# Optimization experiments

Hardware: AMD Instinct MI355X
Metric: run time of the kernel (lower is better)

## Reference

```python
import jax, jax.numpy as jnp
from jax import lax
import numpy as np

DEPTH, SRC, TRG, B, H = 2, 32, 32, 32, 256


def setup_inputs() -> dict:
    key = jax.random.key(0)
    ks = jax.random.split(key, 5)
    s = 1.0 / np.sqrt(H)
    return {
        "source": jax.random.normal(ks[0], (SRC, B, H), jnp.float32),
        "target": jax.random.normal(ks[1], (TRG, B, H), jnp.float32),
        "W": jax.random.uniform(ks[2], (DEPTH, H, H), jnp.float32, -s, s),
        "U": jax.random.uniform(ks[3], (DEPTH, 2 * H, H), jnp.float32, -s, s),
        "b": jax.random.uniform(ks[4], (DEPTH, 1, H), jnp.float32, -s, s),
    }


def _grid_rnn(source, target, W, U, b):
    depth = W.shape[0]
    src_len, batch, hid = source.shape
    trg_len = target.shape[0]
    dt = source.dtype
    # Layer-0 inputs: x_t = source[i] (broadcast over j), y_t = target[j] (broadcast over i)
    x_in = jnp.broadcast_to(source[:, None], (src_len, trg_len, batch, hid))
    y_in = jnp.broadcast_to(target[None, :], (src_len, trg_len, batch, hid))
    outs = []
    for d in range(depth):
        Wd, bd = W[d], b[d]
        Ux, Uy = U[d][:hid], U[d][hid:]  # state = concat([state_x, state_y])
        # Precompute input projections: x_t @ W, y_t @ W for all (i,j)
        Xp = jnp.einsum('ijbh,hk->ijbk', x_in, Wd)
        Yp = jnp.einsum('ijbh,hk->ijbk', y_in, Wd)

        def cell_step(prev_hx, inputs):
            xp, yp, sx = inputs  # sx = h_x from row above (state_x)
            temp = sx @ Ux + prev_hx @ Uy + bd
            hx = jnp.tanh(xp + temp)
            hy = jnp.tanh(yp + temp)
            return hx, (hx, hy)

        def row_step(prev_row_hx, row_in):
            xp_row, yp_row = row_in  # [trg, B, H]
            _, (hx_row, hy_row) = lax.scan(
                cell_step, jnp.zeros((batch, hid), dt), (xp_row, yp_row, prev_row_hx))
            return hx_row, (hx_row, hy_row)

        _, (HX, HY) = lax.scan(row_step, jnp.zeros((trg_len, batch, hid), dt), (Xp, Yp))
        outs.append(jnp.stack([HX, HY], axis=2))  # [src, trg, 2, B, H]
        x_in, y_in = HX, HY  # next layer reads h_output[d-1,i,j,0/1]
    return jnp.stack(outs, 0)  # [depth, src, trg, 2, B, H]


def reference(source, target, W, U, b):
    return _grid_rnn(source, target, W, U, b)
```

## Files before the change

### kernel.cpp

```cpp
#include <hip/hip_runtime.h>
#include <math.h>

#define SRCN 32
#define TRGN 32
#define BN   32
#define HN   256
#define BH   (BN*HN)
#define CELL (2*BH)
#define DSZ  ((size_t)SRCN*TRGN*CELL)
#define NRB  8
#define NBS  4

__host__ __device__ __forceinline__ int ncd(int t) {
    int a = t + 1, b = 63 - t;
    int m = a < b ? a : b;
    return m < 32 ? m : 32;
}

__device__ __forceinline__ void spinwait(int* p) {
    for (int n = 0; n < (1 << 20); ++n) {
        if (__hip_atomic_fetch_add(p, 0, __ATOMIC_RELAXED, __HIP_MEMORY_SCOPE_AGENT) > 0)
            return;
        __builtin_amdgcn_s_sleep(2);
    }
}
__device__ __forceinline__ float cldf(const float* p) {
    return __hip_atomic_load(p, __ATOMIC_RELAXED, __HIP_MEMORY_SCOPE_AGENT);
}
__device__ __forceinline__ void cstf(float* p, float v) {
    __hip_atomic_store(p, v, __ATOMIC_RELAXED, __HIP_MEMORY_SCOPE_AGENT);
}

__global__ __launch_bounds__(256) void proj0_kernel(
    const float* __restrict__ src, const float* __restrict__ trg,
    const float* __restrict__ W0, float* __restrict__ Xp0, float* __restrict__ Yp0)
{
    __shared__ float xs[BH];
    int blk = blockIdx.x >> 2, tile = blockIdx.x & 3;
    const float* X; float* P;
    if (blk < SRCN) { X = src + blk * BH; P = Xp0 + blk * BH; }
    else            { X = trg + (blk - SRCN) * BH; P = Yp0 + (blk - SRCN) * BH; }
    int tid = threadIdx.x;
    { const float4* x4 = (const float4*)X; float4* s4 = (float4*)xs;
#pragma unroll
      for (int r = 0; r < 8; ++r) s4[tid + r * 256] = x4[tid + r * 256]; }
    __syncthreads();
    int h = tile * 64 + (tid & 63), bg = tid >> 6;
    float acc[8] = {0,0,0,0,0,0,0,0};
    for (int k = 0; k < HN; k += 4) {
        float w0 = W0[(k+0)*HN+h], w1 = W0[(k+1)*HN+h], w2 = W0[(k+2)*HN+h], w3 = W0[(k+3)*HN+h];
#pragma unroll
        for (int bb = 0; bb < 8; ++bb) {
            int b = bg * 8 + bb;
            float4 xv = *(const float4*)&xs[b * HN + k];
            acc[bb] += xv.x*w0 + xv.y*w1 + xv.z*w2 + xv.w*w3;
        }
    }
#pragma unroll
    for (int bb = 0; bb < 8; ++bb) P[(bg*8+bb)*HN + h] = acc[bb];
}

__global__ __launch_bounds__(512, 1) void chain3_kernel(
    const float* __restrict__ W, const float* __restrict__ U,
    const float* __restrict__ bias, float* __restrict__ out,
    const float* __restrict__ xp0, const float* __restrict__ yp0,
    int* __restrict__ flg)
{
    __shared__ __align__(16) float sPrev[NRB][HN];
    __shared__ __align__(16) float sUp[NRB][HN];
    __shared__ __align__(16) float sX0[NRB][HN];
    __shared__ __align__(16) float sY0[NRB][HN];
    __shared__ __align__(16) float redT[NRB][HN];
    __shared__ __align__(16) float redX[NRB][HN];
    __shared__ __align__(16) float redY[NRB][HN];

    const int blk = blockIdx.x;
    const int L   = blk >> 7;
    const int i   = (blk >> 2) & 31;
    const int bs  = blk & (NBS - 1);
    const int r0  = bs * NRB;
    const int tid = threadIdx.x;
    const int h   = tid & 255;
    const int kh  = tid >> 8;
    const int kof = kh * 128;

    const float* UxB = U + (size_t)L * 131072 + (size_t)kof * HN + h;
    const float* UyB = UxB + 65536;
    const float* W1B = W + 65536 + (size_t)kof * HN + h;
    const float bv   = bias[L * HN + h];
    float* outL = out + (size_t)L * DSZ;
    int* flgL   = flg + L * 4096;

#pragma unroll
    for (int bb = 0; bb < 4; ++bb) sPrev[kh * 4 + bb][h] = 0.f;
    __syncthreads();

    for (int j = 0; j < TRGN; ++j) {
        const int cell = i * TRGN + j;

        if (L == 1) {
            if (tid == 0) spinwait(&flg[cell * NBS + bs]);
            __syncthreads();
            const float* x0 = out + (size_t)cell * CELL + (size_t)r0 * HN + h;
#pragma unroll
            for (int bb = 0; bb < 4; ++bb) {
                int b = kh * 4 + bb;
                sX0[b][h] = cldf(x0 + b * HN);
                sY0[b][h] = cldf(x0 + BH + b * HN);
            }
            __syncthreads();
        }

        float acc[NRB] = {0.f,0.f,0.f,0.f,0.f,0.f,0.f,0.f};
        if (j > 0) {
#pragma unroll 2
            for (int k = 0; k < 128; k += 4) {
                float w0 = UyB[(k+0)*HN], w1 = UyB[(k+1)*HN];
                float w2 = UyB[(k+2)*HN], w3 = UyB[(k+3)*HN];
#pragma unroll
                for (int b = 0; b < NRB; ++b) {
                    float4 s = *(const float4*)&sPrev[b][kof + k];
                    acc[b] += s.x*w0 + s.y*w1 + s.z*w2 + s.w*w3;
                }
            }
        }
        float aX[NRB] = {0.f,0.f,0.f,0.f,0.f,0.f,0.f,0.f};
        float aY[NRB] = {0.f,0.f,0.f,0.f,0.f,0.f,0.f,0.f};
        float xin[NRB], yin[NRB];
        if (L == 1) {
#pragma unroll 2
            for (int k = 0; k < 128; k += 4) {
                float w0 = W1B[(k+0)*HN], w1 = W1B[(k+1)*HN];
                float w2 = W1B[(k+2)*HN], w3 = W1B[(k+3)*HN];
#pragma unroll
                for (int b = 0; b < NRB; ++b) {
                    float4 sx4 = *(const float4*)&sX0[b][kof + k];
                    float4 sy4 = *(const float4*)&sY0[b][kof + k];
                    aX[b] += sx4.x*w0 + sx4.y*w1 + sx4.z*w2 + sx4.w*w3;
                    aY[b] += sy4.x*w0 + sy4.y*w1 + sy4.z*w2 + sy4.w*w3;
                }
            }
        } else if (kh == 0) {
            const float* xr = xp0 + (size_t)i * BH + (size_t)r0 * HN + h;
            const float* yr = yp0 + (size_t)j * BH + (size_t)r0 * HN + h;
#pragma unroll
            for (int b = 0; b < NRB; ++b) {
                xin[b] = xr[b * HN];
                yin[b] = yr[b * HN];
            }
        }

        if (tid == 0 && i > 0) spinwait(&flgL[((i - 1) * 32 + j) * NBS + bs]);
        __syncthreads();
        if (i > 0) {
            const float* up = outL + (size_t)((i - 1) * TRGN + j) * CELL
                            + (size_t)r0 * HN + h;
#pragma unroll
            for (int bb = 0; bb < 4; ++bb) {
                int b = kh * 4 + bb;
                sUp[b][h] = cldf(up + b * HN);
            }
            __syncthreads();
#pragma unroll 2
            for (int k = 0; k < 128; k += 4) {
                float w0 = UxB[(k+0)*HN], w1 = UxB[(k+1)*HN];
                float w2 = UxB[(k+2)*HN], w3 = UxB[(k+3)*HN];
#pragma unroll
                for (int b = 0; b < NRB; ++b) {
                    float4 s = *(const float4*)&sUp[b][kof + k];
                    acc[b] += s.x*w0 + s.y*w1 + s.z*w2 + s.w*w3;
                }
            }
        }

        if (kh == 1) {
#pragma unroll
            for (int b = 0; b < NRB; ++b) {
                redT[b][h] = acc[b];
                if (L == 1) { redX[b][h] = aX[b]; redY[b][h] = aY[b]; }
            }
        }
        __syncthreads();

        float temp[NRB];
        if (kh == 0) {
            float* ox = outL + (size_t)cell * CELL + (size_t)r0 * HN + h;
            if (L == 0) {
#pragma unroll
                for (int b = 0; b < NRB; ++b) {
                    float tp = acc[b] + redT[b][h] + bv;
                    float hx = tanhf(xin[b] + tp);
                    float hy = tanhf(yin[b] + tp);
                    cstf(ox + b * HN, hx);
                    cstf(ox + BH + b * HN, hy);
                    sPrev[b][h] = hx;
                }
            } else {
#pragma unroll
                for (int b = 0; b < NRB; ++b) {
                    float tp = acc[b] + redT[b][h] + bv;
                    temp[b] = tp;
                    float hx = tanhf(aX[b] + redX[b][h] + tp);
                    cstf(ox + b * HN, hx);
                    sPrev[b][h] = hx;
                }
            }
        }
        __syncthreads();
        if (tid == 0)
            __hip_atomic_fetch_add(&flgL[cell * NBS + bs], 1,
                                   __ATOMIC_RELEASE, __HIP_MEMORY_SCOPE_AGENT);

        if (L == 1 && kh == 0) {
            float* oy = outL + (size_t)cell * CELL + BH + (size_t)r0 * HN + h;
#pragma unroll
            for (int b = 0; b < NRB; ++b)
                oy[b * HN] = tanhf(aY[b] + redY[b][h] + temp[b]);
        }
    }
}

__global__ __launch_bounds__(256) void proj1_kernel(
    float* __restrict__ out, const float* __restrict__ W1)
{
    __shared__ float hxs[BH];
    __shared__ float hys[BH];
    int cell = blockIdx.x >> 2, tile = blockIdx.x & 3;
    const float* hx0 = out + (size_t)cell * CELL;
    const float* hy0 = hx0 + BH;
    float* xp1 = out + DSZ + (size_t)cell * CELL;
    float* yp1 = xp1 + BH;
    int tid = threadIdx.x;
    { const float4* a4 = (const float4*)hx0; const float4* b4 = (const float4*)hy0;
      float4* sa = (float4*)hxs; float4* sb = (float4*)hys;
#pragma unroll
      for (int r = 0; r < 8; ++r) { sa[tid+r*256] = a4[tid+r*256]; sb[tid+r*256] = b4[tid+r*256]; } }
    __syncthreads();
    int h = tile * 64 + (tid & 63), bg = tid >> 6;
    float ax[8] = {0,0,0,0,0,0,0,0}, ay[8] = {0,0,0,0,0,0,0,0};
    for (int k = 0; k < HN; k += 4) {
        float w0 = W1[(k+0)*HN+h], w1 = W1[(k+1)*HN+h], w2 = W1[(k+2)*HN+h], w3 = W1[(k+3)*HN+h];
#pragma unroll
        for (int bb = 0; bb < 8; ++bb) {
            int b = bg * 8 + bb;
            float4 xv = *(const float4*)&hxs[b*HN+k];
            float4 yv = *(const float4*)&hys[b*HN+k];
            ax[bb] += xv.x*w0 + xv.y*w1 + xv.z*w2 + xv.w*w3;
            ay[bb] += yv.x*w0 + yv.y*w1 + yv.z*w2 + yv.w*w3;
        }
    }
#pragma unroll
    for (int bb = 0; bb < 8; ++bb) {
        int b = bg * 8 + bb;
        xp1[b*HN+h] = ax[bb]; yp1[b*HN+h] = ay[bb];
    }
}

__global__ __launch_bounds__(256) void diag_kernel(
    float* out, const float* __restrict__ U, const float* __restrict__ bias,
    const float* __restrict__ Xp0, const float* __restrict__ Yp0, int d, int t)
{
    __shared__ float sxs[BH];
    __shared__ float phs[BH];
    int c = blockIdx.x >> 2, tile = blockIdx.x & 3;
    int i0 = t - (TRGN - 1); if (i0 < 0) i0 = 0;
    int i = i0 + c, j = t - i;
    const float* Ux = U + d * (2 * HN * HN);
    const float* Uy = Ux + HN * HN;
    float* outD = out + (size_t)d * DSZ;
    const float* sx = (i > 0) ? outD + (size_t)((i-1)*TRGN + j) * CELL : nullptr;
    const float* ph = (j > 0) ? outD + (size_t)(i*TRGN + (j-1)) * CELL : nullptr;
    float* oHX = outD + (size_t)(i*TRGN + j) * CELL;
    float* oHY = oHX + BH;
    const float* xp = d ? oHX : (Xp0 + i * BH);
    const float* yp = d ? oHY : (Yp0 + j * BH);
    const float* bd = bias + d * HN;
    int tid = threadIdx.x;
    { const float4* s4 = (const float4*)sx; const float4* p4 = (const float4*)ph;
      float4* d1 = (float4*)sxs; float4* d2 = (float4*)phs;
      float4 z = make_float4(0.f,0.f,0.f,0.f);
#pragma unroll
      for (int r = 0; r < 8; ++r) { int idx = tid + r*256; d1[idx] = sx ? s4[idx] : z; d2[idx] = ph ? p4[idx] : z; } }
    __syncthreads();
    int h = tile * 64 + (tid & 63), bg = tid >> 6;
    float acc[8] = {0,0,0,0,0,0,0,0};
    for (int k = 0; k < HN; k += 4) {
        float ux0 = Ux[(k+0)*HN+h], ux1 = Ux[(k+1)*HN+h], ux2 = Ux[(k+2)*HN+h], ux3 = Ux[(k+3)*HN+h];
        float uy0 = Uy[(k+0)*HN+h], uy1 = Uy[(k+1)*HN+h], uy2 = Uy[(k+2)*HN+h], uy3 = Uy[(k+3)*HN+h];
#pragma unroll
        for (int bb = 0; bb < 8; ++bb) {
            int b = bg * 8 + bb;
            float4 sv = *(const float4*)&sxs[b*HN+k];
            float4 pv = *(const float4*)&phs[b*HN+k];
            acc[bb] += sv.x*ux0 + sv.y*ux1 + sv.z*ux2 + sv.w*ux3
                     + pv.x*uy0 + pv.y*uy1 + pv.z*uy2 + pv.w*uy3;
        }
    }
    float bv = bd[h];
#pragma unroll
    for (int bb = 0; bb < 8; ++bb) {
        int b = bg * 8 + bb;
        float temp = acc[bb] + bv;
        oHX[b*HN+h] = tanhf(xp[b*HN+h] + temp);
        oHY[b*HN+h] = tanhf(yp[b*HN+h] + temp);
    }
}

extern "C" void kernel_launch(void* const* d_in, const int* in_sizes, int n_in,
                              void* d_out, int out_size, void* d_ws, size_t ws_size,
                              hipStream_t stream)
{
    const float* source = (const float*)d_in[0];
    const float* target = (const float*)d_in[1];
    const float* W      = (const float*)d_in[2];
    const float* U      = (const float*)d_in[3];
    const float* bias   = (const float*)d_in[4];
    float* out = (float*)d_out;

    const size_t need = 2u * 1024 * 1024 + 32768;
    if (d_ws != nullptr && ws_size >= need) {
        float* xp0 = (float*)d_ws;
        float* yp0 = xp0 + 32 * BH;
        int*   flg = (int*)(yp0 + 32 * BH);
        hipMemsetAsync(flg, 0, 2 * 32 * 32 * NBS * sizeof(int), stream);
        proj0_kernel<<<dim3(64 * 4), dim3(256), 0, stream>>>(source, target, W, xp0, yp0);
        chain3_kernel<<<dim3(2 * 32 * NBS), dim3(512), 0, stream>>>(
            W, U, bias, out, xp0, yp0, flg);
    } else {
        float* Xp0 = out + DSZ;
        float* Yp0 = Xp0 + SRCN * BH;
        proj0_kernel<<<dim3(64 * 4), dim3(256), 0, stream>>>(source, target, W, Xp0, Yp0);
        for (int t = 0; t < SRCN + TRGN - 1; ++t) {
            int nc = ncd(t);
            diag_kernel<<<dim3(nc * 4), dim3(256), 0, stream>>>(out, U, bias, Xp0, Yp0, 0, t);
        }
        proj1_kernel<<<dim3(1024 * 4), dim3(256), 0, stream>>>(out, W + HN * HN);
        for (int t = 0; t < SRCN + TRGN - 1; ++t) {
            int nc = ncd(t);
            diag_kernel<<<dim3(nc * 4), dim3(256), 0, stream>>>(out, U, bias, nullptr, nullptr, 1, t);
        }
    }
}
```

Baseline: 1.582 ms.

## Split layer-1 input projection into dedicated producer blocks in persistent kernel

Adds a third group of 128 blocks that compute the layer-1 input projections (W1 applied to layer-0 hx/hy) per cell and publish them via a new flag array. Layer-1 recurrence blocks then just load the precomputed projections instead of doing the W1 matmul on their critical path. The projection work moves off the serial diagonal chain, at the cost of more resident blocks, an extra round trip through global memory, and another spin-wait per cell.

```diff
diff --git a/kernel.cpp b/kernel.cpp
--- a/kernel.cpp
+++ b/kernel.cpp
@@ -60,56 +60,92 @@
     for (int bb = 0; bb < 8; ++bb) P[(bg*8+bb)*HN + h] = acc[bb];
 }
 
-__global__ __launch_bounds__(512, 1) void chain3_kernel(
+__global__ __launch_bounds__(512, 1) void chain4_kernel(
     const float* __restrict__ W, const float* __restrict__ U,
     const float* __restrict__ bias, float* __restrict__ out,
     const float* __restrict__ xp0, const float* __restrict__ yp0,
     int* __restrict__ flg)
 {
-    __shared__ __align__(16) float sPrev[NRB][HN];
-    __shared__ __align__(16) float sUp[NRB][HN];
-    __shared__ __align__(16) float sX0[NRB][HN];
-    __shared__ __align__(16) float sY0[NRB][HN];
-    __shared__ __align__(16) float redT[NRB][HN];
-    __shared__ __align__(16) float redX[NRB][HN];
-    __shared__ __align__(16) float redY[NRB][HN];
-
-    const int blk = blockIdx.x;
-    const int L   = blk >> 7;
-    const int i   = (blk >> 2) & 31;
-    const int bs  = blk & (NBS - 1);
-    const int r0  = bs * NRB;
-    const int tid = threadIdx.x;
-    const int h   = tid & 255;
-    const int kh  = tid >> 8;
-    const int kof = kh * 128;
-
+    __shared__ __align__(16) float sA[NRB][HN];
+    __shared__ __align__(16) float sB[NRB][HN];
+    __shared__ __align__(16) float sC[NRB][HN];
+    __shared__ __align__(16) float sD[NRB][HN];
+
+    const int role = blockIdx.x >> 7;
+    const int i    = (blockIdx.x >> 2) & 31;
+    const int bs   = blockIdx.x & 3;
+    const int r0   = bs * NRB;
+    const int tid  = threadIdx.x;
+    const int h    = tid & 255;
+    const int kh   = tid >> 8;
+    const int kof  = kh * 128;
+
+    int* flgL0 = flg;
+    int* p1f   = flg + 4096;
+    int* flgL1 = flg + 8192;
+
+    if (role == 1) {
+        const float* W1B = W + 65536 + (size_t)kof * HN + h;
+        for (int j = 0; j < TRGN; ++j) {
+            const int cell = i * TRGN + j;
+            if (tid == 0) spinwait(&flgL0[cell * NBS + bs]);
+            __syncthreads();
+            const float* x0 = out + (size_t)cell * CELL + (size_t)r0 * HN + h;
+#pragma unroll
+            for (int bb = 0; bb < 4; ++bb) {
+                int b = kh * 4 + bb;
+                sA[b][h] = cldf(x0 + b * HN);
+                sB[b][h] = cldf(x0 + BH + b * HN);
+            }
+            __syncthreads();
+            float aX[NRB] = {0.f,0.f,0.f,0.f,0.f,0.f,0.f,0.f};
+            float aY[NRB] = {0.f,0.f,0.f,0.f,0.f,0.f,0.f,0.f};
+#pragma unroll 2
+            for (int k = 0; k < 128; k += 4) {
+                float w0 = W1B[(k+0)*HN], w1 = W1B[(k+1)*HN];
+                float w2 = W1B[(k+2)*HN], w3 = W1B[(k+3)*HN];
+#pragma unroll
+                for (int b = 0; b < NRB; ++b) {
+                    float4 sx4 = *(const float4*)&sA[b][kof + k];
+                    float4 sy4 = *(const float4*)&sB[b][kof + k];
+                    aX[b] += sx4.x*w0 + sx4.y*w1 + sx4.z*w2 + sx4.w*w3;
+                    aY[b] += sy4.x*w0 + sy4.y*w1 + sy4.z*w2 + sy4.w*w3;
+                }
+            }
+            if (kh == 1) {
+#pragma unroll
+                for (int b = 0; b < NRB; ++b) { sC[b][h] = aX[b]; sD[b][h] = aY[b]; }
+            }
+            __syncthreads();
+            if (kh == 0) {
+                float* xd = out + DSZ + (size_t)cell * CELL + (size_t)r0 * HN + h;
+#pragma unroll
+                for (int b = 0; b < NRB; ++b) {
+                    cstf(xd + b * HN,      aX[b] + sC[b][h]);
+                    cstf(xd + BH + b * HN, aY[b] + sD[b][h]);
+                }
+            }
+            __syncthreads();
+            if (tid == 0)
+                __hip_atomic_fetch_add(&p1f[cell * NBS + bs], 1,
+                                       __ATOMIC_RELEASE, __HIP_MEMORY_SCOPE_AGENT);
+        }
+        return;
+    }
+
+    const int L = (role == 2);
     const float* UxB = U + (size_t)L * 131072 + (size_t)kof * HN + h;
     const float* UyB = UxB + 65536;
-    const float* W1B = W + 65536 + (size_t)kof * HN + h;
     const float bv   = bias[L * HN + h];
     float* outL = out + (size_t)L * DSZ;
-    int* flgL   = flg + L * 4096;
-
-#pragma unroll
-    for (int bb = 0; bb < 4; ++bb) sPrev[kh * 4 + bb][h] = 0.f;
+    int* myf    = L ? flgL1 : flgL0;
+
+#pragma unroll
+    for (int bb = 0; bb < 4; ++bb) sA[kh * 4 + bb][h] = 0.f;
     __syncthreads();
 
     for (int j = 0; j < TRGN; ++j) {
         const int cell = i * TRGN + j;
-
-        if (L == 1) {
-            if (tid == 0) spinwait(&flg[cell * NBS + bs]);
-            __syncthreads();
-            const float* x0 = out + (size_t)cell * CELL + (size_t)r0 * HN + h;
-#pragma unroll
-            for (int bb = 0; bb < 4; ++bb) {
-                int b = kh * 4 + bb;
-                sX0[b][h] = cldf(x0 + b * HN);
-                sY0[b][h] = cldf(x0 + BH + b * HN);
-            }
-            __syncthreads();
-        }
 
         float acc[NRB] = {0.f,0.f,0.f,0.f,0.f,0.f,0.f,0.f};
         if (j > 0) {
@@ -119,46 +155,39 @@
                 float w2 = UyB[(k+2)*HN], w3 = UyB[(k+3)*HN];
 #pragma unroll
                 for (int b = 0; b < NRB; ++b) {
-                    float4 s = *(const float4*)&sPrev[b][kof + k];
+                    float4 s = *(const float4*)&sA[b][kof + k];
                     acc[b] += s.x*w0 + s.y*w1 + s.z*w2 + s.w*w3;
                 }
             }
         }
-        float aX[NRB] = {0.f,0.f,0.f,0.f,0.f,0.f,0.f,0.f};
-        float aY[NRB] = {0.f,0.f,0.f,0.f,0.f,0.f,0.f,0.f};
         float xin[NRB], yin[NRB];
-        if (L == 1) {
-#pragma unroll 2
-            for (int k = 0; k < 128; k += 4) {
-                float w0 = W1B[(k+0)*HN], w1 = W1B[(k+1)*HN];
-                float w2 = W1B[(k+2)*HN], w3 = W1B[(k+3)*HN];
-#pragma unroll
-                for (int b = 0; b < NRB; ++b) {
-                    float4 sx4 = *(const float4*)&sX0[b][kof + k];
-                    float4 sy4 = *(const float4*)&sY0[b][kof + k];
-                    aX[b] += sx4.x*w0 + sx4.y*w1 + sx4.z*w2 + sx4.w*w3;
-                    aY[b] += sy4.x*w0 + sy4.y*w1 + sy4.z*w2 + sy4.w*w3;
-                }
-            }
-        } else if (kh == 0) {
+        if (!L && kh == 0) {
             const float* xr = xp0 + (size_t)i * BH + (size_t)r0 * HN + h;
             const float* yr = yp0 + (size_t)j * BH + (size_t)r0 * HN + h;
 #pragma unroll
+            for (int b = 0; b < NRB; ++b) { xin[b] = xr[b * HN]; yin[b] = yr[b * HN]; }
+        }
+
+        if (tid == 0) {
+            if (L)     spinwait(&p1f[cell * NBS + bs]);
+            if (i > 0) spinwait(&myf[((i - 1) * 32 + j) * NBS + bs]);
+        }
+        __syncthreads();
+        if (L && kh == 0) {
+            const float* xd = out + DSZ + (size_t)cell * CELL + (size_t)r0 * HN + h;
+#pragma unroll
             for (int b = 0; b < NRB; ++b) {
-                xin[b] = xr[b * HN];
-                yin[b] = yr[b * HN];
-            }
-        }
-
-        if (tid == 0 && i > 0) spinwait(&flgL[((i - 1) * 32 + j) * NBS + bs]);
-        __syncthreads();
+                xin[b] = cldf(xd + b * HN);
+                yin[b] = cldf(xd + BH + b * HN);
+            }
+        }
         if (i > 0) {
             const float* up = outL + (size_t)((i - 1) * TRGN + j) * CELL
                             + (size_t)r0 * HN + h;
 #pragma unroll
             for (int bb = 0; bb < 4; ++bb) {
                 int b = kh * 4 + bb;
-                sUp[b][h] = cldf(up + b * HN);
+                sB[b][h] = cldf(up + b * HN);
             }
             __syncthreads();
 #pragma unroll 2
@@ -167,7 +196,7 @@
                 float w2 = UxB[(k+2)*HN], w3 = UxB[(k+3)*HN];
 #pragma unroll
                 for (int b = 0; b < NRB; ++b) {
-                    float4 s = *(const float4*)&sUp[b][kof + k];
+                    float4 s = *(const float4*)&sB[b][kof + k];
                     acc[b] += s.x*w0 + s.y*w1 + s.z*w2 + s.w*w3;
                 }
             }
@@ -175,48 +204,26 @@
 
         if (kh == 1) {
 #pragma unroll
-            for (int b = 0; b < NRB; ++b) {
-                redT[b][h] = acc[b];
-                if (L == 1) { redX[b][h] = aX[b]; redY[b][h] = aY[b]; }
-            }
+            for (int b = 0; b < NRB; ++b) sC[b][h] = acc[b];
         }
         __syncthreads();
-
-        float temp[NRB];
         if (kh == 0) {
             float* ox = outL + (size_t)cell * CELL + (size_t)r0 * HN + h;
-            if (L == 0) {
-#pragma unroll
-                for (int b = 0; b < NRB; ++b) {
-                    float tp = acc[b] + redT[b][h] + bv;
-                    float hx = tanhf(xin[b] + tp);
-                    float hy = tanhf(yin[b] + tp);
-                    cstf(ox + b * HN, hx);
-                    cstf(ox + BH + b * HN, hy);
-                    sPrev[b][h] = hx;
-                }
-            } else {
-#pragma unroll
-                for (int b = 0; b < NRB; ++b) {
-                    float tp = acc[b] + redT[b][h] + bv;
-                    temp[b] = tp;
-                    float hx = tanhf(aX[b] + redX[b][h] + tp);
-                    cstf(ox + b * HN, hx);
-                    sPrev[b][h] = hx;
-                }
+#pragma unroll
+            for (int b = 0; b < NRB; ++b) {
+                float tp = acc[b] + sC[b][h] + bv;
+                float hx = tanhf(xin[b] + tp);
+                float hy = tanhf(yin[b] + tp);
+                cstf(ox + b * HN, hx);
+                if (L) ox[BH + b * HN] = hy;
+                else   cstf(ox + BH + b * HN, hy);
+                sA[b][h] = hx;
             }
         }
         __syncthreads();
         if (tid == 0)
-            __hip_atomic_fetch_add(&flgL[cell * NBS + bs], 1,
+            __hip_atomic_fetch_add(&myf[cell * NBS + bs], 1,
                                    __ATOMIC_RELEASE, __HIP_MEMORY_SCOPE_AGENT);
-
-        if (L == 1 && kh == 0) {
-            float* oy = outL + (size_t)cell * CELL + BH + (size_t)r0 * HN + h;
-#pragma unroll
-            for (int b = 0; b < NRB; ++b)
-                oy[b * HN] = tanhf(aY[b] + redY[b][h] + temp[b]);
-        }
     }
 }
 
@@ -317,14 +324,14 @@
     const float* bias   = (const float*)d_in[4];
     float* out = (float*)d_out;
 
-    const size_t need = 2u * 1024 * 1024 + 32768;
+    const size_t need = 2u * 1024 * 1024 + 49152;
     if (d_ws != nullptr && ws_size >= need) {
         float* xp0 = (float*)d_ws;
         float* yp0 = xp0 + 32 * BH;
         int*   flg = (int*)(yp0 + 32 * BH);
-        hipMemsetAsync(flg, 0, 2 * 32 * 32 * NBS * sizeof(int), stream);
+        hipMemsetAsync(flg, 0, 3 * 4096 * sizeof(int), stream);
         proj0_kernel<<<dim3(64 * 4), dim3(256), 0, stream>>>(source, target, W, xp0, yp0);
-        chain3_kernel<<<dim3(2 * 32 * NBS), dim3(512), 0, stream>>>(
+        chain4_kernel<<<dim3(384), dim3(512), 0, stream>>>(
             W, U, bias, out, xp0, yp0, flg);
     } else {
         float* Xp0 = out + DSZ;
```

After: 1.730 ms. 9.4% more time.

## Move layer-1 Y projection into layer-0 blocks and software-pipeline GEMV loads

Applied to the files above, without the earlier changes.

Layer-0 blocks now also compute the W1 projection of their hy output and store it into the layer-1 output slot, signalling a new flag. This takes half of the input-projection work off the layer-1 critical path. Layer-1 blocks no longer load hy or keep redY; they wait on that flag to finish the hy output. A double-buffered register-prefetch GEMV helper replaces the inline loops, and spin waits now happen per wavefront with signal fences instead of through block-wide barriers. The risks are more flag traffic and a possible memory-ordering weakness, since waits use relaxed atomics with only signal fences.

```diff
diff --git a/kernel.cpp b/kernel.cpp
--- a/kernel.cpp
+++ b/kernel.cpp
@@ -31,6 +31,36 @@
     __hip_atomic_store(p, v, __ATOMIC_RELAXED, __HIP_MEMORY_SCOPE_AGENT);
 }
 
+__device__ __forceinline__ void gemm8p(float* acc, const float (*S)[HN], int kof,
+                                       const float* __restrict__ wc)
+{
+    float4 A[NRB], B[NRB];
+#pragma unroll
+    for (int b = 0; b < NRB; ++b) A[b] = *(const float4*)&S[b][kof];
+    for (int k = 0; k < 128; k += 8) {
+#pragma unroll
+        for (int b = 0; b < NRB; ++b) B[b] = *(const float4*)&S[b][kof + k + 4];
+        {
+            float w0 = wc[(k+0)*HN], w1 = wc[(k+1)*HN];
+            float w2 = wc[(k+2)*HN], w3 = wc[(k+3)*HN];
+#pragma unroll
+            for (int b = 0; b < NRB; ++b)
+                acc[b] += A[b].x*w0 + A[b].y*w1 + A[b].z*w2 + A[b].w*w3;
+        }
+        if (k + 8 < 128) {
+#pragma unroll
+            for (int b = 0; b < NRB; ++b) A[b] = *(const float4*)&S[b][kof + k + 8];
+        }
+        {
+            float w0 = wc[(k+4)*HN], w1 = wc[(k+5)*HN];
+            float w2 = wc[(k+6)*HN], w3 = wc[(k+7)*HN];
+#pragma unroll
+            for (int b = 0; b < NRB; ++b)
+                acc[b] += B[b].x*w0 + B[b].y*w1 + B[b].z*w2 + B[b].w*w3;
+        }
+    }
+}
+
 __global__ __launch_bounds__(256) void proj0_kernel(
     const float* __restrict__ src, const float* __restrict__ trg,
     const float* __restrict__ W0, float* __restrict__ Xp0, float* __restrict__ Yp0)
@@ -60,36 +90,39 @@
     for (int bb = 0; bb < 8; ++bb) P[(bg*8+bb)*HN + h] = acc[bb];
 }
 
-__global__ __launch_bounds__(512, 1) void chain3_kernel(
+__global__ __launch_bounds__(512, 1) void chain5_kernel(
     const float* __restrict__ W, const float* __restrict__ U,
     const float* __restrict__ bias, float* __restrict__ out,
     const float* __restrict__ xp0, const float* __restrict__ yp0,
     int* __restrict__ flg)
 {
     __shared__ __align__(16) float sPrev[NRB][HN];
-    __shared__ __align__(16) float sUp[NRB][HN];
-    __shared__ __align__(16) float sX0[NRB][HN];
-    __shared__ __align__(16) float sY0[NRB][HN];
-    __shared__ __align__(16) float redT[NRB][HN];
-    __shared__ __align__(16) float redX[NRB][HN];
-    __shared__ __align__(16) float redY[NRB][HN];
-
-    const int blk = blockIdx.x;
-    const int L   = blk >> 7;
-    const int i   = (blk >> 2) & 31;
-    const int bs  = blk & (NBS - 1);
+    __shared__ __align__(16) float sAux [NRB][HN];
+    __shared__ __align__(16) float sUp  [NRB][HN];
+    __shared__ __align__(16) float redT [NRB][HN];
+    __shared__ __align__(16) float redX [NRB][HN];
+
+    const int bid = blockIdx.x;
+    const int L   = bid >> 7;
+    const int i   = (bid >> 2) & 31;
+    const int bs  = bid & 3;
     const int r0  = bs * NRB;
     const int tid = threadIdx.x;
     const int h   = tid & 255;
     const int kh  = tid >> 8;
     const int kof = kh * 128;
+    const bool k0 = (kh == 0);
+    const bool wl = ((tid & 63) == 0);
+
+    int* fL0 = flg;
+    int* fP1 = flg + 4096;
+    int* fL1 = flg + 8192;
 
     const float* UxB = U + (size_t)L * 131072 + (size_t)kof * HN + h;
     const float* UyB = UxB + 65536;
     const float* W1B = W + 65536 + (size_t)kof * HN + h;
     const float bv   = bias[L * HN + h];
     float* outL = out + (size_t)L * DSZ;
-    int* flgL   = flg + L * 4096;
 
 #pragma unroll
     for (int bb = 0; bb < 4; ++bb) sPrev[kh * 4 + bb][h] = 0.f;
@@ -97,95 +130,34 @@
 
     for (int j = 0; j < TRGN; ++j) {
         const int cell = i * TRGN + j;
-
-        if (L == 1) {
-            if (tid == 0) spinwait(&flg[cell * NBS + bs]);
-            __syncthreads();
-            const float* x0 = out + (size_t)cell * CELL + (size_t)r0 * HN + h;
-#pragma unroll
-            for (int bb = 0; bb < 4; ++bb) {
-                int b = kh * 4 + bb;
-                sX0[b][h] = cldf(x0 + b * HN);
-                sY0[b][h] = cldf(x0 + BH + b * HN);
-            }
-            __syncthreads();
-        }
-
+        const int fidx = cell * NBS + bs;
         float acc[NRB] = {0.f,0.f,0.f,0.f,0.f,0.f,0.f,0.f};
-        if (j > 0) {
-#pragma unroll 2
-            for (int k = 0; k < 128; k += 4) {
-                float w0 = UyB[(k+0)*HN], w1 = UyB[(k+1)*HN];
-                float w2 = UyB[(k+2)*HN], w3 = UyB[(k+3)*HN];
-#pragma unroll
-                for (int b = 0; b < NRB; ++b) {
-                    float4 s = *(const float4*)&sPrev[b][kof + k];
-                    acc[b] += s.x*w0 + s.y*w1 + s.z*w2 + s.w*w3;
-                }
-            }
-        }
-        float aX[NRB] = {0.f,0.f,0.f,0.f,0.f,0.f,0.f,0.f};
-        float aY[NRB] = {0.f,0.f,0.f,0.f,0.f,0.f,0.f,0.f};
-        float xin[NRB], yin[NRB];
-        if (L == 1) {
-#pragma unroll 2
-            for (int k = 0; k < 128; k += 4) {
-                float w0 = W1B[(k+0)*HN], w1 = W1B[(k+1)*HN];
-                float w2 = W1B[(k+2)*HN], w3 = W1B[(k+3)*HN];
-#pragma unroll
-                for (int b = 0; b < NRB; ++b) {
-                    float4 sx4 = *(const float4*)&sX0[b][kof + k];
-                    float4 sy4 = *(const float4*)&sY0[b][kof + k];
-                    aX[b] += sx4.x*w0 + sx4.y*w1 + sx4.z*w2 + sx4.w*w3;
-                    aY[b] += sy4.x*w0 + sy4.y*w1 + sy4.z*w2 + sy4.w*w3;
-                }
-            }
-        } else if (kh == 0) {
-            const float* xr = xp0 + (size_t)i * BH + (size_t)r0 * HN + h;
-            const float* yr = yp0 + (size_t)j * BH + (size_t)r0 * HN + h;
-#pragma unroll
-            for (int b = 0; b < NRB; ++b) {
-                xin[b] = xr[b * HN];
-                yin[b] = yr[b * HN];
-            }
-        }
-
-        if (tid == 0 && i > 0) spinwait(&flgL[((i - 1) * 32 + j) * NBS + bs]);
-        __syncthreads();
-        if (i > 0) {
-            const float* up = outL + (size_t)((i - 1) * TRGN + j) * CELL
-                            + (size_t)r0 * HN + h;
-#pragma unroll
-            for (int bb = 0; bb < 4; ++bb) {
-                int b = kh * 4 + bb;
-                sUp[b][h] = cldf(up + b * HN);
-            }
-            __syncthreads();
-#pragma unroll 2
-            for (int k = 0; k < 128; k += 4) {
-                float w0 = UxB[(k+0)*HN], w1 = UxB[(k+1)*HN];
-                float w2 = UxB[(k+2)*HN], w3 = UxB[(k+3)*HN];
-#pragma unroll
-                for (int b = 0; b < NRB; ++b) {
-                    float4 s = *(const float4*)&sUp[b][kof + k];
-                    acc[b] += s.x*w0 + s.y*w1 + s.z*w2 + s.w*w3;
-                }
-            }
-        }
-
-        if (kh == 1) {
-#pragma unroll
-            for (int b = 0; b < NRB; ++b) {
-                redT[b][h] = acc[b];
-                if (L == 1) { redX[b][h] = aX[b]; redY[b][h] = aY[b]; }
-            }
-        }
-        __syncthreads();
-
-        float temp[NRB];
-        if (kh == 0) {
-            float* ox = outL + (size_t)cell * CELL + (size_t)r0 * HN + h;
-            if (L == 0) {
+
+        if (L == 0) {
+            float xin[NRB], yin[NRB];
+            if (k0) {
+                const float* xr = xp0 + (size_t)i * BH + (size_t)r0 * HN + h;
+                const float* yr = yp0 + (size_t)j * BH + (size_t)r0 * HN + h;
+#pragma unroll
+                for (int b = 0; b < NRB; ++b) { xin[b] = xr[b*HN]; yin[b] = yr[b*HN]; }
+            }
+            if (j > 0) gemm8p(acc, sPrev, kof, UyB);
+            if (i > 0) {
+                if (wl) spinwait(&fL0[fidx - 32 * NBS]);
+                __atomic_signal_fence(__ATOMIC_ACQUIRE);
+                const float* up = outL + (size_t)(cell - 32) * CELL + (size_t)r0 * HN + h;
+#pragma unroll
+                for (int bb = 0; bb < 4; ++bb) { int b = kh*4+bb; sUp[b][h] = cldf(up + b*HN); }
+                __syncthreads();
+                gemm8p(acc, sUp, kof, UxB);
+            }
+            if (kh == 1) {
+#pragma unroll
+                for (int b = 0; b < NRB; ++b) redT[b][h] = acc[b];
+            }
+            __syncthreads();
+            if (k0) {
+                float* ox = outL + (size_t)cell * CELL + (size_t)r0 * HN + h;
 #pragma unroll
                 for (int b = 0; b < NRB; ++b) {
                     float tp = acc[b] + redT[b][h] + bv;
@@ -194,8 +166,57 @@
                     cstf(ox + b * HN, hx);
                     cstf(ox + BH + b * HN, hy);
                     sPrev[b][h] = hx;
+                    sAux[b][h]  = hy;
                 }
-            } else {
+            }
+            __syncthreads();
+            if (tid == 0)
+                __hip_atomic_fetch_add(&fL0[fidx], 1, __ATOMIC_RELEASE, __HIP_MEMORY_SCOPE_AGENT);
+
+            float aY[NRB] = {0.f,0.f,0.f,0.f,0.f,0.f,0.f,0.f};
+            gemm8p(aY, sAux, kof, W1B);
+            if (kh == 1) {
+#pragma unroll
+                for (int b = 0; b < NRB; ++b) redT[b][h] = aY[b];
+            }
+            __syncthreads();
+            if (k0) {
+                float* yd = out + DSZ + (size_t)cell * CELL + BH + (size_t)r0 * HN + h;
+#pragma unroll
+                for (int b = 0; b < NRB; ++b) cstf(yd + b * HN, aY[b] + redT[b][h]);
+            }
+            __syncthreads();
+            if (tid == 0)
+                __hip_atomic_fetch_add(&fP1[fidx], 1, __ATOMIC_RELEASE, __HIP_MEMORY_SCOPE_AGENT);
+        } else {
+            if (wl) spinwait(&fL0[fidx]);
+            __atomic_signal_fence(__ATOMIC_ACQUIRE);
+            {
+                const float* x0 = out + (size_t)cell * CELL + (size_t)r0 * HN + h;
+#pragma unroll
+                for (int bb = 0; bb < 4; ++bb) { int b = kh*4+bb; sAux[b][h] = cldf(x0 + b*HN); }
+            }
+            __syncthreads();
+            if (j > 0) gemm8p(acc, sPrev, kof, UyB);
+            float aX[NRB] = {0.f,0.f,0.f,0.f,0.f,0.f,0.f,0.f};
+            gemm8p(aX, sAux, kof, W1B);
+            if (i > 0) {
+                if (wl) spinwait(&fL1[fidx - 32 * NBS]);
+                __atomic_signal_fence(__ATOMIC_ACQUIRE);
+                const float* up = outL + (size_t)(cell - 32) * CELL + (size_t)r0 * HN + h;
+#pragma unroll
+                for (int bb = 0; bb < 4; ++bb) { int b = kh*4+bb; sUp[b][h] = cldf(up + b*HN); }
+                __syncthreads();
+                gemm8p(acc, sUp, kof, UxB);
+            }
+            if (kh == 1) {
+#pragma unroll
+                for (int b = 0; b < NRB; ++b) { redT[b][h] = acc[b]; redX[b][h] = aX[b]; }
+            }
+            __syncthreads();
+            float temp[NRB];
+            if (k0) {
+                float* ox = outL + (size_t)cell * CELL + (size_t)r0 * HN + h;
 #pragma unroll
                 for (int b = 0; b < NRB; ++b) {
                     float tp = acc[b] + redT[b][h] + bv;
@@ -205,17 +226,20 @@
                     sPrev[b][h] = hx;
                 }
             }
-        }
-        __syncthreads();
-        if (tid == 0)
-            __hip_atomic_fetch_add(&flgL[cell * NBS + bs], 1,
-                                   __ATOMIC_RELEASE, __HIP_MEMORY_SCOPE_AGENT);
-
-        if (L == 1 && kh == 0) {
-            float* oy = outL + (size_t)cell * CELL + BH + (size_t)r0 * HN + h;
-#pragma unroll
-            for (int b = 0; b < NRB; ++b)
-                oy[b * HN] = tanhf(aY[b] + redY[b][h] + temp[b]);
+            __syncthreads();
+            if (tid == 0)
+                __hip_atomic_fetch_add(&fL1[fidx], 1, __ATOMIC_RELEASE, __HIP_MEMORY_SCOPE_AGENT);
+
+            if (k0) {
+                if (wl) spinwait(&fP1[fidx]);
+                __atomic_signal_fence(__ATOMIC_ACQUIRE);
+                float* oy = outL + (size_t)cell * CELL + BH + (size_t)r0 * HN + h;
+#pragma unroll
+                for (int b = 0; b < NRB; ++b) {
+                    float yp = cldf(oy + b * HN);
+                    oy[b * HN] = tanhf(yp + temp[b]);
+                }
+            }
         }
     }
 }
@@ -317,14 +341,14 @@
     const float* bias   = (const float*)d_in[4];
     float* out = (float*)d_out;
 
-    const size_t need = 2u * 1024 * 1024 + 32768;
+    const size_t need = 2u * 1024 * 1024 + 49152;
     if (d_ws != nullptr && ws_size >= need) {
         float* xp0 = (float*)d_ws;
         float* yp0 = xp0 + 32 * BH;
         int*   flg = (int*)(yp0 + 32 * BH);
-        hipMemsetAsync(flg, 0, 2 * 32 * 32 * NBS * sizeof(int), stream);
+        hipMemsetAsync(flg, 0, 3 * 4096 * sizeof(int), stream);
         proj0_kernel<<<dim3(64 * 4), dim3(256), 0, stream>>>(source, target, W, xp0, yp0);
-        chain3_kernel<<<dim3(2 * 32 * NBS), dim3(512), 0, stream>>>(
+        chain5_kernel<<<dim3(256), dim3(512), 0, stream>>>(
             W, U, bias, out, xp0, yp0, flg);
     } else {
         float* Xp0 = out + DSZ;
```

Result: faster. 1.469 ms (-7.1%).
